# Kernel optimization log

Measured on AMD Instinct MI355X. Metric: run time of the kernel, lower is better.

## Reference

```python
import jax, jax.numpy as jnp
import numpy as np

N = 50000      # nodes
E = 600000     # edges
DIN = 128      # dim_in
DOUT = 128     # dim_out (mulhead=1)
DG = 64        # dim_gate


def setup_inputs() -> dict:
    key = jax.random.key(0)
    ks = jax.random.split(key, 10)
    rows = jax.random.randint(ks[0], (E,), 0, N, dtype=jnp.int32)   # dest nodes
    cols = jax.random.randint(ks[1], (E,), 0, N, dtype=jnp.int32)   # src nodes
    vals = jax.random.uniform(ks[2], (E,), dtype=jnp.float32)       # adj_norm values
    feat = jax.random.normal(ks[3], (N, DIN), dtype=jnp.float32)
    s = 1.0 / np.sqrt(DIN)
    W0 = jax.random.normal(ks[4], (DIN, DOUT), dtype=jnp.float32) * s
    b0 = jnp.zeros((DOUT,), dtype=jnp.float32)
    W1 = jax.random.normal(ks[5], (DIN, DOUT), dtype=jnp.float32) * s
    b1 = jnp.zeros((DOUT,), dtype=jnp.float32)
    att = jax.random.normal(ks[6], (2 * DOUT,), dtype=jnp.float32) * 0.1  # attention param [1, 2*DOUT] flattened
    W_pool = jax.random.normal(ks[7], (DIN, DG), dtype=jnp.float32) * s    # weight_pool_gate
    W_gate = jax.random.normal(ks[8], (2 * DIN + DG, 1), dtype=jnp.float32) * 0.05  # weight_gate, mulhead=1
    offset0 = jnp.zeros((DOUT,), dtype=jnp.float32)
    scale0 = jnp.ones((DOUT,), dtype=jnp.float32)
    offset1 = jnp.zeros((DOUT,), dtype=jnp.float32)
    scale1 = jnp.ones((DOUT,), dtype=jnp.float32)
    return dict(rows=rows, cols=cols, vals=vals, feat=feat, W0=W0, b0=b0,
                W1=W1, b1=b1, att=att, W_pool=W_pool, W_gate=W_gate,
                offset0=offset0, scale0=scale0, offset1=offset1, scale1=scale1)


def _batch_norm(x, scale, offset):
    # per-node norm over the feature dim (unbiased=False), matching _batch_norm
    m = x.mean(axis=1, keepdims=True)
    v = x.var(axis=1, keepdims=True) + 1e-9
    return (x - m) * scale * jax.lax.rsqrt(v) + offset


def reference(rows, cols, vals, feat, W0, b0, W1, b1, att, W_pool, W_gate,
              offset0, scale0, offset1, scale1):
    n = feat.shape[0]
    d = W0.shape[1]
    # --- gate value (GaAN eq. 3) ---
    zj = feat @ W_pool                                   # [N, DG]
    neigh_zj = jax.ops.segment_max(zj[cols], rows, num_segments=n)  # per-row max over neighbors
    neigh_zj = jnp.where(jnp.isfinite(neigh_zj), neigh_zj, 0.0)     # empty rows -> zeros
    neigh_mean = jax.ops.segment_sum(vals[:, None] * feat[cols], rows, num_segments=n)  # spmm(adj, feat)
    gate = jnp.concatenate([feat, neigh_zj, neigh_mean], axis=1) @ W_gate  # [N, 1]
    # --- per-order feature transforms (order=1, mulhead=1) ---
    h0 = jax.nn.relu(feat @ W0 + b0)                     # order 0 (self)
    h1 = jax.nn.relu(feat @ W1 + b1)                     # order 1 (neighbor)
    # --- sparse attention aggregation ---
    a_self = jax.nn.leaky_relu(h0 @ att[:d], 0.2)        # [N]
    a_neigh = jax.nn.leaky_relu(h1 @ att[d:], 0.2)       # [N]
    e = a_self[rows] + a_neigh[cols]                     # per-edge score (replaces adj values)
    agg = jax.ops.segment_sum(e[:, None] * h1[cols], rows, num_segments=n)  # spmm(att_adj, h1)
    agg = agg * gate[:, :1]                              # gated
    # --- per-node batch norm, then 'mean' aggregation (sum of orders) ---
    return _batch_norm(h0, scale0, offset0) + _batch_norm(agg, scale1, offset1)
```

## Files before the change

kernel.cpp:

```cpp
#include <hip/hip_runtime.h>

#define DIN 128
#define DG 64

typedef __attribute__((ext_vector_type(8))) short short8;
typedef __attribute__((ext_vector_type(4))) float f32x4;

static __device__ __forceinline__ unsigned short f2bf(float x) {
    unsigned u = __builtin_bit_cast(unsigned, x);
    u = (u + 0x7FFF + ((u >> 16) & 1)) >> 16;
    return (unsigned short)u;
}
static __device__ __forceinline__ float bf2f(unsigned short s) {
    return __builtin_bit_cast(float, (unsigned)s << 16);
}

__global__ void k_pre(const int* __restrict__ rows, int* __restrict__ deg,
                      int* __restrict__ slot, int E, int nDeg,
                      const float* __restrict__ W0, const float* __restrict__ W1,
                      unsigned short* __restrict__ Bt) {
    int b = blockIdx.x;
    if (b < nDeg) {
        int e = b * 256 + threadIdx.x;
        if (e < E) slot[e] = atomicAdd(&deg[rows[e]], 1);
    } else {
        int k = b - nDeg;
        int c = threadIdx.x;
        const float* W = (c < 128) ? W0 : W1;
        Bt[c * 128 + k] = f2bf(W[k * 128 + (c & 127)]);
    }
}

#define AS_LD 132
#define ALD 136
#define SMEM_BYTES 25088

static __device__ __forceinline__ void zj_body(
    const float* __restrict__ feat, const float* __restrict__ Wp,
    const float* __restrict__ Wg,
    float* __restrict__ zj, float* __restrict__ gpart, float* __restrict__ fdotg,
    int N, char* smem) {
    float* As = (float*)smem;
    float* Bs = (float*)(smem + 32 * AS_LD * 4);
    int tid = threadIdx.x;
    int tx = tid & 15, ty = tid >> 4;
    int m0 = blockIdx.x * 128;
    if (m0 >= N) return;
    float acc[8][4];
    #pragma unroll
    for (int r = 0; r < 8; ++r)
        #pragma unroll
        for (int c = 0; c < 4; ++c) acc[r][c] = 0.f;
    float gdot[8], fdot[8];
    #pragma unroll
    for (int r = 0; r < 8; ++r) { gdot[r] = 0.f; fdot[r] = 0.f; }
    for (int kc = 0; kc < 128; kc += 32) {
        for (int i = tid; i < 1024; i += 256) {
            int m = i >> 3, kq = (i & 7) << 2;
            int node = m0 + m;
            float4 f;
            if (node < N) f = *(const float4*)&feat[(size_t)node * 128 + kc + kq];
            else          f = make_float4(0.f, 0.f, 0.f, 0.f);
            As[(kq + 0) * AS_LD + m] = f.x;
            As[(kq + 1) * AS_LD + m] = f.y;
            As[(kq + 2) * AS_LD + m] = f.z;
            As[(kq + 3) * AS_LD + m] = f.w;
        }
        for (int i = tid; i < 512; i += 256) {
            int k = i >> 4, cq = (i & 15) << 2;
            *(float4*)&Bs[k * 64 + cq] = *(const float4*)&Wp[(size_t)(kc + k) * 64 + cq];
        }
        __syncthreads();
        #pragma unroll 8
        for (int kk = 0; kk < 32; ++kk) {
            const float* ar = &As[kk * AS_LD];
            float4 a0 = *(const float4*)(ar + 4 * tx);
            float4 a1 = *(const float4*)(ar + 64 + 4 * tx);
            float4 b0v = *(const float4*)&Bs[kk * 64 + 4 * ty];
            float a[8] = {a0.x, a0.y, a0.z, a0.w, a1.x, a1.y, a1.z, a1.w};
            #pragma unroll
            for (int r = 0; r < 8; ++r) {
                acc[r][0] += a[r] * b0v.x; acc[r][1] += a[r] * b0v.y;
                acc[r][2] += a[r] * b0v.z; acc[r][3] += a[r] * b0v.w;
            }
            float g1 = Wg[kc + kk];
            float g2 = Wg[192 + kc + kk];
            #pragma unroll
            for (int r = 0; r < 8; ++r) { gdot[r] += a[r] * g1; fdot[r] += a[r] * g2; }
        }
        __syncthreads();
    }
    #pragma unroll
    for (int r = 0; r < 8; ++r) {
        int node = m0 + ((r < 4) ? (4 * tx + r) : (64 + 4 * tx + (r - 4)));
        if (node >= N) continue;
        *(float4*)&zj[(size_t)node * 64 + 4 * ty] =
            make_float4(acc[r][0], acc[r][1], acc[r][2], acc[r][3]);
        if (ty == 0) { gpart[node] = gdot[r]; fdotg[node] = fdot[r]; }
    }
}

static __device__ __forceinline__ void mfma_body(
    const float* __restrict__ feat, const unsigned short* __restrict__ Bt,
    const float* __restrict__ b0, const float* __restrict__ b1,
    const float* __restrict__ att,
    float* __restrict__ h0, unsigned short* __restrict__ hb,
    float* __restrict__ a_self, float* __restrict__ a_neigh, int N, char* smem) {
    unsigned short* As = (unsigned short*)smem;
    float* sredA = (float*)(smem + 64 * ALD * 2);
    float* nredA = sredA + 128;
    int tid = threadIdx.x;
    int m0 = blockIdx.x * 64;
    for (int i = tid; i < 2048; i += 256) {
        int row = i >> 5, ch = i & 31;
        int node = m0 + row;
        float4 f;
        if (node < N) f = *(const float4*)&feat[(size_t)node * 128 + ch * 4];
        else          f = make_float4(0.f, 0.f, 0.f, 0.f);
        unsigned p0 = (unsigned)f2bf(f.x) | ((unsigned)f2bf(f.y) << 16);
        unsigned p1 = (unsigned)f2bf(f.z) | ((unsigned)f2bf(f.w) << 16);
        *(uint2*)&As[row * ALD + ch * 4] = make_uint2(p0, p1);
    }
    __syncthreads();
    int w = tid >> 6, lane = tid & 63;
    int lm = lane & 15, q = lane >> 4;
    f32x4 acc[4][4];
    #pragma unroll
    for (int rt = 0; rt < 4; ++rt)
        #pragma unroll
        for (int ct = 0; ct < 4; ++ct)
            #pragma unroll
            for (int r = 0; r < 4; ++r) acc[rt][ct][r] = 0.f;
    #pragma unroll
    for (int ks = 0; ks < 4; ++ks) {
        short8 a[4], b[4];
        #pragma unroll
        for (int rt = 0; rt < 4; ++rt)
            a[rt] = *(const short8*)&As[(rt * 16 + lm) * ALD + ks * 32 + q * 8];
        #pragma unroll
        for (int ct = 0; ct < 4; ++ct)
            b[ct] = *(const short8*)&Bt[(size_t)(w * 64 + ct * 16 + lm) * 128 + ks * 32 + q * 8];
        #pragma unroll
        for (int rt = 0; rt < 4; ++rt)
            #pragma unroll
            for (int ct = 0; ct < 4; ++ct)
                acc[rt][ct] = __builtin_amdgcn_mfma_f32_16x16x32_bf16(a[rt], b[ct], acc[rt][ct], 0, 0, 0);
    }
    float sacc[4][4];
    #pragma unroll
    for (int rt = 0; rt < 4; ++rt)
        #pragma unroll
        for (int r = 0; r < 4; ++r) sacc[rt][r] = 0.f;
    #pragma unroll
    for (int ct = 0; ct < 4; ++ct) {
        int col = w * 64 + ct * 16 + lm;
        float attc = att[col];
        float bias = (w < 2) ? b0[col] : b1[col - 128];
        #pragma unroll
        for (int rt = 0; rt < 4; ++rt) {
            #pragma unroll
            for (int r = 0; r < 4; ++r) {
                float v = acc[rt][ct][r] + bias;
                v = fmaxf(v, 0.f);
                sacc[rt][r] += v * attc;
                int node = m0 + rt * 16 + q * 4 + r;
                if (node < N) {
                    if (w < 2) h0[(size_t)node * 128 + col] = v;
                    else       hb[(size_t)node * 128 + (col - 128)] = f2bf(v);
                }
            }
        }
    }
    float* red = (w < 2) ? sredA : nredA;
    #pragma unroll
    for (int rt = 0; rt < 4; ++rt)
        #pragma unroll
        for (int r = 0; r < 4; ++r) {
            float s = sacc[rt][r];
            s += __shfl_xor(s, 1, 64); s += __shfl_xor(s, 2, 64);
            s += __shfl_xor(s, 4, 64); s += __shfl_xor(s, 8, 64);
            if (lm == 0) red[(w & 1) * 64 + rt * 16 + q * 4 + r] = s;
        }
    __syncthreads();
    if (tid < 64) {
        int node = m0 + tid;
        if (node < N) {
            float s  = sredA[tid] + sredA[64 + tid];
            float nn = nredA[tid] + nredA[64 + tid];
            a_self[node]  = (s  >= 0.f) ? s  : 0.2f * s;
            a_neigh[node] = (nn >= 0.f) ? nn : 0.2f * nn;
        }
    }
}

static __device__ __forceinline__ void scan_body(
    const int* __restrict__ deg, int* __restrict__ rowptr,
    unsigned long long* __restrict__ bstate, int n, int nbs, char* smem) {
    int b = blockIdx.x;
    if (b >= nbs) return;
    int* wsum = (int*)smem;
    int* bprefs = (int*)smem + 8;
    int tid = threadIdx.x, lane = tid & 63, w = tid >> 6;
    int base = b * 1024 + tid * 4;
    int4 v = make_int4(0, 0, 0, 0);
    if (base + 3 < n) v = *(const int4*)&deg[base];
    else {
        if (base     < n) v.x = deg[base];
        if (base + 1 < n) v.y = deg[base + 1];
        if (base + 2 < n) v.z = deg[base + 2];
        if (base + 3 < n) v.w = deg[base + 3];
    }
    int s = v.x + v.y + v.z + v.w;
    int x = s;
    #pragma unroll
    for (int off = 1; off < 64; off <<= 1) {
        int y = __shfl_up(x, off, 64);
        if (lane >= off) x += y;
    }
    if (lane == 63) wsum[w] = x;
    __syncthreads();
    int wpref = 0;
    for (int t = 0; t < w; ++t) wpref += wsum[t];
    int btotal = wsum[0] + wsum[1] + wsum[2] + wsum[3];
    int excl = x - s + wpref;
    if (tid == 0) {
        unsigned long long pack =
            ((unsigned long long)(b == 0 ? 2u : 1u) << 32) | (unsigned)btotal;
        atomicExch(&bstate[b], pack);
        int pref = 0;
        if (b > 0) {
            int i = b - 1;
            while (i >= 0) {
                unsigned long long st = atomicAdd(&bstate[i], 0ULL);
                unsigned f = (unsigned)(st >> 32);
                if (f == 0) { __builtin_amdgcn_s_sleep(1); continue; }
                pref += (int)(st & 0xffffffffULL);
                if (f == 2) break;
                --i;
            }
            atomicExch(&bstate[b], (2ULL << 32) | (unsigned)(pref + btotal));
        }
        bprefs[0] = pref;
    }
    __syncthreads();
    int p = bprefs[0] + excl;
    if (base + 3 < n) {
        *(int4*)&rowptr[base] = make_int4(p, p + v.x, p + v.x + v.y, p + v.x + v.y + v.z);
    } else {
        if (base     < n) rowptr[base]     = p;
        if (base + 1 < n) rowptr[base + 1] = p + v.x;
        if (base + 2 < n) rowptr[base + 2] = p + v.x + v.y;
        if (base + 3 < n) rowptr[base + 3] = p + v.x + v.y + v.z;
    }
    if (b == nbs - 1 && tid == 0) rowptr[n] = bprefs[0] + btotal;
}

__global__ __launch_bounds__(256) void k_fused(
    const float* __restrict__ feat, const float* __restrict__ Wp,
    const unsigned short* __restrict__ Bt,
    const float* __restrict__ b0, const float* __restrict__ b1,
    const float* __restrict__ att, const float* __restrict__ Wg,
    float* __restrict__ h0, unsigned short* __restrict__ hb,
    float* __restrict__ zj, float* __restrict__ gpart, float* __restrict__ fdotg,
    float* __restrict__ a_self, float* __restrict__ a_neigh,
    const int* __restrict__ deg, int* __restrict__ rowptr,
    unsigned long long* __restrict__ bstate, int nbs, int N) {
    __shared__ __align__(16) char smem[SMEM_BYTES];
    if (blockIdx.y == 0)
        zj_body(feat, Wp, Wg, zj, gpart, fdotg, N, smem);
    else if (blockIdx.y == 1)
        mfma_body(feat, Bt, b0, b1, att, h0, hb, a_self, a_neigh, N, smem);
    else
        scan_body(deg, rowptr, bstate, N, nbs, smem);
}

__global__ void k_scatter_meta(const int* __restrict__ rows, const int* __restrict__ cols,
                               const float* __restrict__ vals,
                               const int* __restrict__ rowptr, const int* __restrict__ slot,
                               const float* __restrict__ a_neigh, const float* __restrict__ fdotg,
                               float4* __restrict__ meta, int E) {
    int e = blockIdx.x * blockDim.x + threadIdx.x;
    if (e < E) {
        int c = cols[e];
        int dst = rowptr[rows[e]] + slot[e];
        meta[dst] = make_float4(__builtin_bit_cast(float, c),
                                a_neigh[c], vals[e] * fdotg[c], 0.f);
    }
}

template<int C>
static __device__ __forceinline__ void agg_chunk_m(
    const float4* __restrict__ meta, int j, int je, int lane, float asr,
    const unsigned short* __restrict__ hb, const float* __restrict__ zj,
    float2& acca, float& zmax, float& vfsum) {
    int jclamp = (je > 0) ? (je - 1) : 0;
    float4 m[C]; bool act[C];
    #pragma unroll
    for (int t = 0; t < C; ++t) {
        int jj = j + t;
        act[t] = jj < je;
        m[t] = meta[act[t] ? jj : jclamp];
    }
    ushort2 hv[C]; float zv[C];
    #pragma unroll
    for (int t = 0; t < C; ++t) {
        int c = __builtin_bit_cast(int, m[t].x);
        hv[t] = ((const ushort2*)(hb + (size_t)c * 128))[lane];
        zv[t] = zj[(size_t)c * 64 + lane];
    }
    #pragma unroll
    for (int t = 0; t < C; ++t) {
        float es = act[t] ? (asr + m[t].y) : 0.f;
        acca.x += es * bf2f(hv[t].x);
        acca.y += es * bf2f(hv[t].y);
        zmax = fmaxf(zmax, act[t] ? zv[t] : -__builtin_inff());
        vfsum += act[t] ? m[t].z : 0.f;
    }
}

__global__ __launch_bounds__(256) void k_aggregate(
    const float4* __restrict__ meta, const int* __restrict__ rowptr,
    const float* __restrict__ h0, const unsigned short* __restrict__ hb,
    const float* __restrict__ zj,
    const float* __restrict__ a_self, const float* __restrict__ gpart,
    const float* __restrict__ Wg,
    const float* __restrict__ scale0, const float* __restrict__ offset0,
    const float* __restrict__ scale1, const float* __restrict__ offset1,
    float* __restrict__ out, int N) {
    int r = blockIdx.x * 4 + (threadIdx.x >> 6);
    int lane = threadIdx.x & 63;
    if (r >= N) return;
    int jb = rowptr[r], je = rowptr[r + 1];
    float2 acca = {0.f, 0.f};
    float zmax = -__builtin_inff();
    float vfsum = 0.f;
    float asr = a_self[r];
    for (int j = jb; j < je; j += 8)
        agg_chunk_m<8>(meta, j, je, lane, asr, hb, zj, acca, zmax, vfsum);
    if (jb == je) zmax = 0.f;
    float gs = zmax * Wg[128 + lane];
    #pragma unroll
    for (int off = 32; off; off >>= 1) gs += __shfl_xor(gs, off, 64);
    float gate = gpart[r] + gs + vfsum;
    float2 ag = {acca.x * gate, acca.y * gate};
    float2 x0 = ((const float2*)(h0 + (size_t)r * 128))[lane];
    float m0s = x0.x + x0.y;
    #pragma unroll
    for (int off = 32; off; off >>= 1) m0s += __shfl_xor(m0s, off, 64);
    float m0 = m0s * (1.f / 128.f);
    float d0x = x0.x - m0, d0y = x0.y - m0;
    float v0s = d0x * d0x + d0y * d0y;
    #pragma unroll
    for (int off = 32; off; off >>= 1) v0s += __shfl_xor(v0s, off, 64);
    float inv0 = rsqrtf(v0s * (1.f / 128.f) + 1e-9f);
    float m1s = ag.x + ag.y;
    #pragma unroll
    for (int off = 32; off; off >>= 1) m1s += __shfl_xor(m1s, off, 64);
    float m1 = m1s * (1.f / 128.f);
    float d1x = ag.x - m1, d1y = ag.y - m1;
    float v1s = d1x * d1x + d1y * d1y;
    #pragma unroll
    for (int off = 32; off; off >>= 1) v1s += __shfl_xor(v1s, off, 64);
    float inv1 = rsqrtf(v1s * (1.f / 128.f) + 1e-9f);
    float2 sc0 = ((const float2*)scale0)[lane], of0 = ((const float2*)offset0)[lane];
    float2 sc1 = ((const float2*)scale1)[lane], of1 = ((const float2*)offset1)[lane];
    float2 o;
    o.x = d0x * sc0.x * inv0 + of0.x + d1x * sc1.x * inv1 + of1.x;
    o.y = d0y * sc0.y * inv0 + of0.y + d1y * sc1.y * inv1 + of1.y;
    ((float2*)(out + (size_t)r * 128))[lane] = o;
}

extern "C" void kernel_launch(void* const* d_in, const int* in_sizes, int n_in,
                              void* d_out, int out_size, void* d_ws, size_t ws_size,
                              hipStream_t stream) {
    const int*   rows   = (const int*)d_in[0];
    const int*   cols   = (const int*)d_in[1];
    const float* vals   = (const float*)d_in[2];
    const float* feat   = (const float*)d_in[3];
    const float* W0     = (const float*)d_in[4];
    const float* b0     = (const float*)d_in[5];
    const float* W1     = (const float*)d_in[6];
    const float* b1     = (const float*)d_in[7];
    const float* att    = (const float*)d_in[8];
    const float* Wp     = (const float*)d_in[9];
    const float* Wg     = (const float*)d_in[10];
    const float* offset0 = (const float*)d_in[11];
    const float* scale0  = (const float*)d_in[12];
    const float* offset1 = (const float*)d_in[13];
    const float* scale1  = (const float*)d_in[14];
    float* out = (float*)d_out;

    const int E = in_sizes[0];
    const int N = in_sizes[3] / DIN;
    const int Npad = (N + 63) & ~63;

    char* ws = (char*)d_ws;
    float* h0          = (float*)ws;          ws += (size_t)N * 128 * sizeof(float);
    unsigned short* hb = (unsigned short*)ws; ws += (size_t)N * 128 * sizeof(unsigned short);
    float* zj          = (float*)ws;          ws += (size_t)N * 64 * sizeof(float);
    unsigned short* Bt = (unsigned short*)ws; ws += (size_t)256 * 128 * sizeof(unsigned short);
    float* a_self  = (float*)ws; ws += (size_t)N * sizeof(float);
    float* a_neigh = (float*)ws; ws += (size_t)N * sizeof(float);
    float* gpart   = (float*)ws; ws += (size_t)N * sizeof(float);
    float* fdotg   = (float*)ws; ws += (size_t)N * sizeof(float);
    ws = (char*)(((size_t)ws + 7) & ~(size_t)7);
    unsigned long long* bstate = (unsigned long long*)ws; ws += 64 * sizeof(unsigned long long);
    int* deg      = (int*)ws; ws += (size_t)(N + 1) * sizeof(int);
    int* rowptr   = (int*)ws; ws += (size_t)(N + 1) * sizeof(int);
    int* slot     = (int*)ws; ws += (size_t)E * sizeof(int);
    ws = (char*)(((size_t)ws + 15) & ~(size_t)15);
    float4* meta  = (float4*)ws; ws += (size_t)E * sizeof(float4);

    hipMemsetAsync(bstate, 0, 64 * sizeof(unsigned long long) + (size_t)(N + 1) * sizeof(int), stream);

    int nDeg = (E + 255) / 256;
    k_pre<<<nDeg + 128, 256, 0, stream>>>(rows, deg, slot, E, nDeg, W0, W1, Bt);

    int nbs = (N + 1023) >> 10;
    dim3 gg(Npad / 64, 3);
    k_fused<<<gg, 256, 0, stream>>>(feat, Wp, Bt, b0, b1, att, Wg,
                                    h0, hb, zj, gpart, fdotg, a_self, a_neigh,
                                    deg, rowptr, bstate, nbs, N);

    k_scatter_meta<<<nDeg, 256, 0, stream>>>(rows, cols, vals, rowptr, slot,
                                             a_neigh, fdotg, meta, E);

    int nb4 = (N + 3) / 4;
    k_aggregate<<<nb4, 256, 0, stream>>>(meta, rowptr, h0, hb, zj,
                                         a_self, gpart, Wg,
                                         scale0, offset0, scale1, offset1, out, N);
}
```

Measured before the change: 247.8 us.

## Interleave bf16 h1 and zj into one 512-byte packed row per node

Source-node data used in aggregation, the bf16 h1 row and the fp32 zj row, is interleaved into a single 512-byte record per node. Each lane then fetches both pieces with one 16-byte load per edge instead of two separate gathers. The aggregate kernel now processes two rows per wavefront, 32 lanes each, with float4 accesses. The meta column index is pre-shifted to a byte offset. The cost is scattered 2-byte stores in the MFMA epilogue and wasted lanes when the two half-wave rows have unequal degree.

```diff
diff --git a/kernel.cpp b/kernel.cpp
--- a/kernel.cpp
+++ b/kernel.cpp
@@ -14,6 +14,13 @@
 static __device__ __forceinline__ float bf2f(unsigned short s) {
     return __builtin_bit_cast(float, (unsigned)s << 16);
 }
+static __device__ __forceinline__ float bflo(unsigned u) {
+    return __builtin_bit_cast(float, u << 16);
+}
+static __device__ __forceinline__ float bfhi(unsigned u) {
+    return __builtin_bit_cast(float, u & 0xFFFF0000u);
+}
+
 
 __global__ void k_pre(const int* __restrict__ rows, int* __restrict__ deg,
                       int* __restrict__ slot, int E, int nDeg,
@@ -38,7 +45,7 @@
 static __device__ __forceinline__ void zj_body(
     const float* __restrict__ feat, const float* __restrict__ Wp,
     const float* __restrict__ Wg,
-    float* __restrict__ zj, float* __restrict__ gpart, float* __restrict__ fdotg,
+    char* __restrict__ pack, float* __restrict__ gpart, float* __restrict__ fdotg,
     int N, char* smem) {
     float* As = (float*)smem;
     float* Bs = (float*)(smem + 32 * AS_LD * 4);
@@ -94,8 +101,9 @@
     for (int r = 0; r < 8; ++r) {
         int node = m0 + ((r < 4) ? (4 * tx + r) : (64 + 4 * tx + (r - 4)));
         if (node >= N) continue;
-        *(float4*)&zj[(size_t)node * 64 + 4 * ty] =
-            make_float4(acc[r][0], acc[r][1], acc[r][2], acc[r][3]);
+        char* rb = pack + (size_t)node * 512 + (size_t)ty * 32 + 8;
+        *(float2*)(rb)      = make_float2(acc[r][0], acc[r][1]);
+        *(float2*)(rb + 16) = make_float2(acc[r][2], acc[r][3]);
         if (ty == 0) { gpart[node] = gdot[r]; fdotg[node] = fdot[r]; }
     }
 }
@@ -104,7 +112,7 @@
     const float* __restrict__ feat, const unsigned short* __restrict__ Bt,
     const float* __restrict__ b0, const float* __restrict__ b1,
     const float* __restrict__ att,
-    float* __restrict__ h0, unsigned short* __restrict__ hb,
+    float* __restrict__ h0, char* __restrict__ pack,
     float* __restrict__ a_self, float* __restrict__ a_neigh, int N, char* smem) {
     unsigned short* As = (unsigned short*)smem;
     float* sredA = (float*)(smem + 64 * ALD * 2);
@@ -156,6 +164,8 @@
         int col = w * 64 + ct * 16 + lm;
         float attc = att[col];
         float bias = (w < 2) ? b0[col] : b1[col - 128];
+        int cp = col - 128;
+        int pofs = ((cp >> 2) * 16 + (cp & 3) * 2);
         #pragma unroll
         for (int rt = 0; rt < 4; ++rt) {
             #pragma unroll
@@ -166,7 +176,7 @@
                 int node = m0 + rt * 16 + q * 4 + r;
                 if (node < N) {
                     if (w < 2) h0[(size_t)node * 128 + col] = v;
-                    else       hb[(size_t)node * 128 + (col - 128)] = f2bf(v);
+                    else       *(unsigned short*)(pack + (size_t)node * 512 + pofs) = f2bf(v);
                 }
             }
         }
@@ -260,16 +270,16 @@
     const unsigned short* __restrict__ Bt,
     const float* __restrict__ b0, const float* __restrict__ b1,
     const float* __restrict__ att, const float* __restrict__ Wg,
-    float* __restrict__ h0, unsigned short* __restrict__ hb,
-    float* __restrict__ zj, float* __restrict__ gpart, float* __restrict__ fdotg,
+    float* __restrict__ h0, char* __restrict__ pack,
+    float* __restrict__ gpart, float* __restrict__ fdotg,
     float* __restrict__ a_self, float* __restrict__ a_neigh,
     const int* __restrict__ deg, int* __restrict__ rowptr,
     unsigned long long* __restrict__ bstate, int nbs, int N) {
     __shared__ __align__(16) char smem[SMEM_BYTES];
     if (blockIdx.y == 0)
-        zj_body(feat, Wp, Wg, zj, gpart, fdotg, N, smem);
+        zj_body(feat, Wp, Wg, pack, gpart, fdotg, N, smem);
     else if (blockIdx.y == 1)
-        mfma_body(feat, Bt, b0, b1, att, h0, hb, a_self, a_neigh, N, smem);
+        mfma_body(feat, Bt, b0, b1, att, h0, pack, a_self, a_neigh, N, smem);
     else
         scan_body(deg, rowptr, bstate, N, nbs, smem);
 }
@@ -283,91 +293,96 @@
     if (e < E) {
         int c = cols[e];
         int dst = rowptr[rows[e]] + slot[e];
-        meta[dst] = make_float4(__builtin_bit_cast(float, c),
+        meta[dst] = make_float4(__builtin_bit_cast(float, c << 9),
                                 a_neigh[c], vals[e] * fdotg[c], 0.f);
-    }
-}
-
-template<int C>
-static __device__ __forceinline__ void agg_chunk_m(
-    const float4* __restrict__ meta, int j, int je, int lane, float asr,
-    const unsigned short* __restrict__ hb, const float* __restrict__ zj,
-    float2& acca, float& zmax, float& vfsum) {
-    int jclamp = (je > 0) ? (je - 1) : 0;
-    float4 m[C]; bool act[C];
-    #pragma unroll
-    for (int t = 0; t < C; ++t) {
-        int jj = j + t;
-        act[t] = jj < je;
-        m[t] = meta[act[t] ? jj : jclamp];
-    }
-    ushort2 hv[C]; float zv[C];
-    #pragma unroll
-    for (int t = 0; t < C; ++t) {
-        int c = __builtin_bit_cast(int, m[t].x);
-        hv[t] = ((const ushort2*)(hb + (size_t)c * 128))[lane];
-        zv[t] = zj[(size_t)c * 64 + lane];
-    }
-    #pragma unroll
-    for (int t = 0; t < C; ++t) {
-        float es = act[t] ? (asr + m[t].y) : 0.f;
-        acca.x += es * bf2f(hv[t].x);
-        acca.y += es * bf2f(hv[t].y);
-        zmax = fmaxf(zmax, act[t] ? zv[t] : -__builtin_inff());
-        vfsum += act[t] ? m[t].z : 0.f;
     }
 }
 
 __global__ __launch_bounds__(256) void k_aggregate(
     const float4* __restrict__ meta, const int* __restrict__ rowptr,
-    const float* __restrict__ h0, const unsigned short* __restrict__ hb,
-    const float* __restrict__ zj,
+    const float* __restrict__ h0, const char* __restrict__ pack,
     const float* __restrict__ a_self, const float* __restrict__ gpart,
     const float* __restrict__ Wg,
     const float* __restrict__ scale0, const float* __restrict__ offset0,
     const float* __restrict__ scale1, const float* __restrict__ offset1,
     float* __restrict__ out, int N) {
-    int r = blockIdx.x * 4 + (threadIdx.x >> 6);
+    int wid = threadIdx.x >> 6;
     int lane = threadIdx.x & 63;
+    int sub = lane >> 5;
+    int l = lane & 31;
+    int r = blockIdx.x * 8 + wid * 2 + sub;
+    int rr = (r < N) ? r : (N - 1);
+    int jb = rowptr[rr], je = rowptr[rr + 1];
+    int trips = (je - jb + 7) >> 3;
+    int tother = __shfl_xor(trips, 32, 64);
+    int tmax = (trips > tother) ? trips : tother;
+    int jclamp = (je > 0) ? je - 1 : 0;
+    float asr = a_self[rr];
+    const char* packl = pack + l * 16;
+    float4 acc = make_float4(0.f, 0.f, 0.f, 0.f);
+    float2 zmax = make_float2(-__builtin_inff(), -__builtin_inff());
+    float vfsum = 0.f;
+    for (int t0 = 0; t0 < tmax; ++t0) {
+        int j = jb + t0 * 8;
+        int joff[8]; float esv[8];
+        #pragma unroll
+        for (int t = 0; t < 8; ++t) {
+            int jj = j + t;
+            bool a = jj < je;
+            float4 mt = meta[a ? jj : jclamp];
+            joff[t] = __builtin_bit_cast(int, mt.x);
+            esv[t] = a ? (asr + mt.y) : 0.f;
+            vfsum += a ? mt.z : 0.f;
+        }
+        uint4 v[8];
+        #pragma unroll
+        for (int t = 0; t < 8; ++t)
+            v[t] = *(const uint4*)(packl + (size_t)(unsigned)joff[t]);
+        #pragma unroll
+        for (int t = 0; t < 8; ++t) {
+            float e = esv[t];
+            acc.x += e * bflo(v[t].x);
+            acc.y += e * bfhi(v[t].x);
+            acc.z += e * bflo(v[t].y);
+            acc.w += e * bfhi(v[t].y);
+            zmax.x = fmaxf(zmax.x, __builtin_bit_cast(float, v[t].z));
+            zmax.y = fmaxf(zmax.y, __builtin_bit_cast(float, v[t].w));
+        }
+    }
+    if (jb == je) { zmax.x = 0.f; zmax.y = 0.f; }
+    float gs = zmax.x * Wg[128 + 2 * l] + zmax.y * Wg[129 + 2 * l];
+    #pragma unroll
+    for (int off = 16; off; off >>= 1) gs += __shfl_xor(gs, off, 64);
+    float gate = gpart[rr] + gs + vfsum;
+    float4 ag = make_float4(acc.x * gate, acc.y * gate, acc.z * gate, acc.w * gate);
+    float4 x0 = ((const float4*)(h0 + (size_t)rr * 128))[l];
+    float m0s = x0.x + x0.y + x0.z + x0.w;
+    #pragma unroll
+    for (int off = 16; off; off >>= 1) m0s += __shfl_xor(m0s, off, 64);
+    float m0 = m0s * (1.f / 128.f);
+    float4 d0 = make_float4(x0.x - m0, x0.y - m0, x0.z - m0, x0.w - m0);
+    float v0s = d0.x * d0.x + d0.y * d0.y + d0.z * d0.z + d0.w * d0.w;
+    #pragma unroll
+    for (int off = 16; off; off >>= 1) v0s += __shfl_xor(v0s, off, 64);
+    float inv0 = rsqrtf(v0s * (1.f / 128.f) + 1e-9f);
+    float m1s = ag.x + ag.y + ag.z + ag.w;
+    #pragma unroll
+    for (int off = 16; off; off >>= 1) m1s += __shfl_xor(m1s, off, 64);
+    float m1 = m1s * (1.f / 128.f);
+    float4 d1 = make_float4(ag.x - m1, ag.y - m1, ag.z - m1, ag.w - m1);
+    float v1s = d1.x * d1.x + d1.y * d1.y + d1.z * d1.z + d1.w * d1.w;
+    #pragma unroll
+    for (int off = 16; off; off >>= 1) v1s += __shfl_xor(v1s, off, 64);
+    float inv1 = rsqrtf(v1s * (1.f / 128.f) + 1e-9f);
     if (r >= N) return;
-    int jb = rowptr[r], je = rowptr[r + 1];
-    float2 acca = {0.f, 0.f};
-    float zmax = -__builtin_inff();
-    float vfsum = 0.f;
-    float asr = a_self[r];
-    for (int j = jb; j < je; j += 8)
-        agg_chunk_m<8>(meta, j, je, lane, asr, hb, zj, acca, zmax, vfsum);
-    if (jb == je) zmax = 0.f;
-    float gs = zmax * Wg[128 + lane];
-    #pragma unroll
-    for (int off = 32; off; off >>= 1) gs += __shfl_xor(gs, off, 64);
-    float gate = gpart[r] + gs + vfsum;
-    float2 ag = {acca.x * gate, acca.y * gate};
-    float2 x0 = ((const float2*)(h0 + (size_t)r * 128))[lane];
-    float m0s = x0.x + x0.y;
-    #pragma unroll
-    for (int off = 32; off; off >>= 1) m0s += __shfl_xor(m0s, off, 64);
-    float m0 = m0s * (1.f / 128.f);
-    float d0x = x0.x - m0, d0y = x0.y - m0;
-    float v0s = d0x * d0x + d0y * d0y;
-    #pragma unroll
-    for (int off = 32; off; off >>= 1) v0s += __shfl_xor(v0s, off, 64);
-    float inv0 = rsqrtf(v0s * (1.f / 128.f) + 1e-9f);
-    float m1s = ag.x + ag.y;
-    #pragma unroll
-    for (int off = 32; off; off >>= 1) m1s += __shfl_xor(m1s, off, 64);
-    float m1 = m1s * (1.f / 128.f);
-    float d1x = ag.x - m1, d1y = ag.y - m1;
-    float v1s = d1x * d1x + d1y * d1y;
-    #pragma unroll
-    for (int off = 32; off; off >>= 1) v1s += __shfl_xor(v1s, off, 64);
-    float inv1 = rsqrtf(v1s * (1.f / 128.f) + 1e-9f);
-    float2 sc0 = ((const float2*)scale0)[lane], of0 = ((const float2*)offset0)[lane];
-    float2 sc1 = ((const float2*)scale1)[lane], of1 = ((const float2*)offset1)[lane];
-    float2 o;
-    o.x = d0x * sc0.x * inv0 + of0.x + d1x * sc1.x * inv1 + of1.x;
-    o.y = d0y * sc0.y * inv0 + of0.y + d1y * sc1.y * inv1 + of1.y;
-    ((float2*)(out + (size_t)r * 128))[lane] = o;
+    float4 sc0 = ((const float4*)scale0)[l], of0 = ((const float4*)offset0)[l];
+    float4 sc1 = ((const float4*)scale1)[l], of1 = ((const float4*)offset1)[l];
+    float4 o;
+    o.x = d0.x * sc0.x * inv0 + of0.x + d1.x * sc1.x * inv1 + of1.x;
+    o.y = d0.y * sc0.y * inv0 + of0.y + d1.y * sc1.y * inv1 + of1.y;
+    o.z = d0.z * sc0.z * inv0 + of0.z + d1.z * sc1.z * inv1 + of1.z;
+    o.w = d0.w * sc0.w * inv0 + of0.w + d1.w * sc1.w * inv1 + of1.w;
+    ((float4*)(out + (size_t)r * 128))[l] = o;
 }
 
 extern "C" void kernel_launch(void* const* d_in, const int* in_sizes, int n_in,
@@ -396,8 +411,7 @@
 
     char* ws = (char*)d_ws;
     float* h0          = (float*)ws;          ws += (size_t)N * 128 * sizeof(float);
-    unsigned short* hb = (unsigned short*)ws; ws += (size_t)N * 128 * sizeof(unsigned short);
-    float* zj          = (float*)ws;          ws += (size_t)N * 64 * sizeof(float);
+    char* pack         = ws;                  ws += (size_t)N * 512;
     unsigned short* Bt = (unsigned short*)ws; ws += (size_t)256 * 128 * sizeof(unsigned short);
     float* a_self  = (float*)ws; ws += (size_t)N * sizeof(float);
     float* a_neigh = (float*)ws; ws += (size_t)N * sizeof(float);
@@ -419,14 +433,14 @@
     int nbs = (N + 1023) >> 10;
     dim3 gg(Npad / 64, 3);
     k_fused<<<gg, 256, 0, stream>>>(feat, Wp, Bt, b0, b1, att, Wg,
-                                    h0, hb, zj, gpart, fdotg, a_self, a_neigh,
+                                    h0, pack, gpart, fdotg, a_self, a_neigh,
                                     deg, rowptr, bstate, nbs, N);
 
     k_scatter_meta<<<nDeg, 256, 0, stream>>>(rows, cols, vals, rowptr, slot,
                                              a_neigh, fdotg, meta, E);
 
-    int nb4 = (N + 3) / 4;
-    k_aggregate<<<nb4, 256, 0, stream>>>(meta, rowptr, h0, hb, zj,
+    int nb8 = (N + 7) / 8;
+    k_aggregate<<<nb8, 256, 0, stream>>>(meta, rowptr, h0, pack,
                                          a_self, gpart, Wg,
                                          scale0, offset0, scale1, offset1, out, N);
 }
```

Result: no change. 250.2 us (+1.0%).
